# Performance work log

Measured on AMD Instinct MI355X. Metric: run time of the kernel, lower is better.

Reference implementation:

```python
import jax, jax.numpy as jnp
import numpy as np

NUM_HEADS = 12
ROPE_THETA = 100.0

def _rotate_half(x):
    x1 = x[..., ::2]
    x2 = x[..., 1::2]
    return jnp.stack((-x2, x1), axis=-1).reshape(x.shape)

def _apply_rope(x, cos, sin):
    return x * cos + _rotate_half(x) * sin

def _rope_cos_sin(h, w, head_dim, theta):
    quarter = head_dim // 4  # head_dim=64 -> 16 freq bands
    inv_freq = 1.0 / theta ** (jnp.arange(quarter, dtype=jnp.float32) / max(quarter, 1))
    y = jnp.repeat(jnp.arange(h, dtype=jnp.float32), w)   # [h*w]
    xc = jnp.tile(jnp.arange(w, dtype=jnp.float32), h)    # [h*w]
    y_freqs = y[:, None] * inv_freq[None, :]               # [N, quarter]
    x_freqs = xc[:, None] * inv_freq[None, :]
    y_ang = jnp.repeat(y_freqs, 2, axis=-1)                # [N, half]
    x_ang = jnp.repeat(x_freqs, 2, axis=-1)
    ang = jnp.concatenate([y_ang, x_ang], axis=-1)         # [N, head_dim]
    return jnp.cos(ang)[None, None], jnp.sin(ang)[None, None]  # [1,1,N,hd]

def setup_inputs() -> dict:
    key = jax.random.key(0)
    ks = jax.random.split(key, 8)
    B, S, D = 8, 1025, 768
    s = 0.02
    return {
        "x": jax.random.normal(ks[0], (B, S, D), jnp.float32),
        "q_w": jax.random.normal(ks[1], (D, D), jnp.float32) * s,
        "q_b": jax.random.normal(ks[2], (D,), jnp.float32) * s,
        "k_w": jax.random.normal(ks[3], (D, D), jnp.float32) * s,
        "v_w": jax.random.normal(ks[4], (D, D), jnp.float32) * s,
        "v_b": jax.random.normal(ks[5], (D,), jnp.float32) * s,
        "o_w": jax.random.normal(ks[6], (D, D), jnp.float32) * s,
        "o_b": jax.random.normal(ks[7], (D,), jnp.float32) * s,
        "h": 32,
        "w": 32,
        "num_prefix_tokens": 1,
    }

def reference(x, q_w, q_b, k_w, v_w, v_b, o_w, o_b, h, w, num_prefix_tokens):
    B, S, D = x.shape
    H = NUM_HEADS
    hd = D // H
    scale = hd ** -0.5
    p = num_prefix_tokens

    def proj(W, b):
        y = jnp.einsum('bsd,ed->bse', x, W)
        if b is not None:
            y = y + b
        return y.reshape(B, S, H, hd).transpose(0, 2, 1, 3)  # [B,H,S,hd]

    q = proj(q_w, q_b)
    k = proj(k_w, None)
    v = proj(v_w, v_b)

    cos, sin = _rope_cos_sin(h, w, hd, ROPE_THETA)
    q = jnp.concatenate([q[:, :, :p], _apply_rope(q[:, :, p:], cos, sin)], axis=2)
    k = jnp.concatenate([k[:, :, :p], _apply_rope(k[:, :, p:], cos, sin)], axis=2)

    attn = jnp.einsum('bhqd,bhkd->bhqk', q * scale, k)
    attn = jax.nn.softmax(attn, axis=-1)
    out = jnp.einsum('bhqk,bhkd->bhqd', attn, v)
    out = out.transpose(0, 2, 1, 3).reshape(B, S, D)
    return jnp.einsum('bsd,ed->bse', out, o_w) + o_b
```

## Files before the change

kernel.cpp:

```cpp
#include <hip/hip_runtime.h>

typedef unsigned short u16;
typedef unsigned int   u32;
typedef __attribute__((ext_vector_type(4))) short s4;
typedef __attribute__((ext_vector_type(8))) short s8;
typedef __attribute__((ext_vector_type(4))) float f4;
typedef __attribute__((ext_vector_type(16))) float f16v;

#define NB   8
#define SEQ  1025
#define DIM  768
#define NH   12
#define HD   64
#define BPAD 1040
#define MPAD 8320
#define MV   8200
#define SQP  1040
#define SKP  1088
#define NG16 68
#define NQKV 2304
#define BHT  96
#define QSCALE 0.1803368801111204f

__device__ __forceinline__ u16 f2bf(float f) {
  u32 u = __builtin_bit_cast(u32, f);
  u += 0x7fffu + ((u >> 16) & 1u);
  return (u16)(u >> 16);
}
__device__ __forceinline__ float bf2f(u16 h) {
  return __builtin_bit_cast(float, ((u32)h) << 16);
}
__device__ __forceinline__ float exp2f_(float x) {
#if __has_builtin(__builtin_amdgcn_exp2f)
  return __builtin_amdgcn_exp2f(x);
#else
  return exp2f(x);
#endif
}
__device__ __forceinline__ u32 cvtpk(float a, float b) {
  u32 r;
  asm("v_cvt_pk_bf16_f32 %0, %1, %2" : "=v"(r) : "v"(a), "v"(b));
  return r;
}

typedef const __attribute__((address_space(1))) void cas1v;
typedef __attribute__((address_space(3))) void as3v;
__device__ __forceinline__ void gload16(const void* g, void* l) {
  __builtin_amdgcn_global_load_lds((cas1v*)g, (as3v*)l, 16, 0, 0);
}

#define MFMA16(a, b, c) __builtin_amdgcn_mfma_f32_16x16x32_bf16(a, b, c, 0, 0, 0)
#define MFMA32(a, b, c) __builtin_amdgcn_mfma_f32_32x32x16_bf16(a, b, c, 0, 0, 0)

__global__ void conv_all(const float* __restrict__ x,
                         const float* __restrict__ qw, const float* __restrict__ kw,
                         const float* __restrict__ vw, const float* __restrict__ ow,
                         const float* __restrict__ qb, const float* __restrict__ vb,
                         u16* __restrict__ xb,
                         u16* __restrict__ wqkv, u16* __restrict__ wo,
                         float* __restrict__ biasq, float2* __restrict__ rt) {
  if (blockIdx.x < 6240) {
    int i = blockIdx.x * 256 + threadIdx.x;
    int e = i * 4;
    int row = e / DIM, col = e - row * DIM;
    int b = row / BPAD, s = row - b * BPAD;
    s4 o;
    if (s < SEQ) {
      float4 v = *(const float4*)(x + ((size_t)(b * SEQ + s)) * DIM + col);
      o[0] = (short)f2bf(v.x); o[1] = (short)f2bf(v.y);
      o[2] = (short)f2bf(v.z); o[3] = (short)f2bf(v.w);
    } else {
      o = (s4){0, 0, 0, 0};
    }
    *(s4*)(xb + e) = o;
  } else {
    int i = (blockIdx.x - 6240) * 256 + threadIdx.x;
    wqkv[i]           = f2bf(qw[i]);
    wqkv[i + 589824]  = f2bf(kw[i]);
    wqkv[i + 1179648] = f2bf(vw[i]);
    wo[i]             = f2bf(ow[i]);
    if (i < NQKV) biasq[i] = (i < 768) ? qb[i] : (i < 1536 ? 0.f : vb[i - 1536]);
    if (i < SEQ * 32) {
      int s = i >> 5, jj = i & 31;
      float cs = 1.f, sn = 0.f;
      if (s > 0) {
        int tok = s - 1;
        int pos = (jj < 16) ? (tok >> 5) : (tok & 31);
        int f = jj & 15;
        float ang = (float)pos * __expf((float)f * -0.28782313662425572f);
        __sincosf(ang, &sn, &cs);
      }
      rt[i] = make_float2(cs, sn);
    }
  }
}

__global__ __launch_bounds__(512, 4) void gemm_qkv(const u16* __restrict__ A, const u16* __restrict__ Bm,
                                                   const float* __restrict__ bias,
                                                   u16* __restrict__ Ql, u16* __restrict__ Kl,
                                                   u16* __restrict__ Vp, const float2* __restrict__ rt) {
  __shared__ u16 smem[24576];
  const int K = DIM;
  int tid = threadIdx.x;
  int lane = tid & 63, wave = tid >> 6;
  int g = lane >> 4, c16 = lane & 15;
  int wm = wave >> 2, wn = wave & 3;
  int nwg = gridDim.x, orig = blockIdx.x;
  int qd = nwg >> 3, rm = nwg & 7, xcd = orig & 7;
  int wgid = (xcd < rm ? xcd * (qd + 1) : rm * (qd + 1) + (xcd - rm) * qd) + (orig >> 3);
  int m0 = (wgid / 9) * 128, n0 = (wgid % 9) * 256;
  f4 acc[4][4] = {};

  int ldrow = wave * 16 + (lane >> 2);
  int ldk = ((lane & 3) ^ ((ldrow >> 1) & 3)) * 8;
  const u16* Asrc = A + (size_t)(m0 + ldrow) * K + ldk;
  const u16* Bsrc = Bm + (size_t)(n0 + ldrow) * K + ldk;

  auto stage = [&](int buf, int k0) {
    gload16(Asrc + k0,           smem + buf * 4096 + wave * 512);
    gload16(Bsrc + k0,           smem + 8192 + buf * 8192 + wave * 512);
    gload16(Bsrc + 128 * K + k0, smem + 8192 + buf * 8192 + 4096 + wave * 512);
  };

  stage(0, 0);
  __syncthreads();
  int kx = (g ^ ((c16 >> 1) & 3)) * 8;
  for (int t = 0; t < 24; t++) {
    int buf = t & 1;
    if (t + 1 < 24) stage(buf ^ 1, (t + 1) << 5);
    s8 af[4], bf[4];
#pragma unroll
    for (int i = 0; i < 4; i++) {
      af[i] = *(const s8*)(smem + buf * 4096 + (wm * 64 + i * 16 + c16) * 32 + kx);
      bf[i] = *(const s8*)(smem + 8192 + buf * 8192 + (wn * 64 + i * 16 + c16) * 32 + kx);
    }
    __builtin_amdgcn_s_setprio(1);
#pragma unroll
    for (int i = 0; i < 4; i++)
#pragma unroll
      for (int j = 0; j < 4; j++)
        acc[i][j] = MFMA16(af[i], bf[j], acc[i][j]);
    __builtin_amdgcn_s_setprio(0);
    __syncthreads();
  }

  int part = (n0 >= 1536) ? 2 : (n0 >= 768 ? 1 : 0);
  float qs = (part == 0) ? QSCALE : 1.0f;
  u16 (*ct)[258] = (u16(*)[258])smem;
#pragma unroll
  for (int ih = 0; ih < 2; ih++) {
    __syncthreads();
#pragma unroll
    for (int j = 0; j < 4; j++) {
      int col = wn * 64 + j * 16 + c16;
      float bv = bias[n0 + col];
      int jj = (col & 63) >> 1;
      int odd = col & 1;
#pragma unroll
      for (int il = 0; il < 2; il++) {
        int i = ih * 2 + il;
        int lrow = wm * 32 + il * 16 + g * 4;
        int mrow = m0 + wm * 64 + i * 16 + g * 4;
#pragma unroll
        for (int r = 0; r < 4; r++) {
          float v = acc[i][j][r] + bv;
          u16 o;
          if (part < 2) {
            float vp = __shfl_xor(v, 1);
            int s = (mrow + r) % BPAD;
            float2 t = rt[(s < SEQ ? s : SEQ - 1) * 32 + jj];
            float rv = odd ? (v * t.x + vp * t.y) : (v * t.x - vp * t.y);
            o = f2bf(rv * qs);
          } else {
            o = f2bf(v);
          }
          ct[lrow + r][col] = o;
        }
      }
    }
    __syncthreads();
    if (part < 2) {
      u16* dstB = (part == 0) ? Ql : Kl;
      int stride = (part == 0) ? SQP : SKP;
#pragma unroll
      for (int p = 0; p < 4; p++) {
        int task = p * 512 + tid;
        int lrow = task >> 5, cg = (task & 31) * 8;
        int m = m0 + (lrow >> 5) * 64 + ih * 32 + (lrow & 31);
        int b = m / BPAD, s = m - b * BPAD;
        int n = n0 + cg;
        int hq = (n >> 6) - part * NH;
        s8 v = *(const s8*)&ct[lrow][cg];
        *(s8*)(dstB + ((size_t)((b * NH + hq) * stride + s)) * HD + (n & 63)) = v;
      }
    } else {
#pragma unroll
      for (int p = 0; p < 2; p++) {
        int task = p * 512 + tid;
        int col = task & 255, rg = task >> 8;
        int lbase = rg * 16;
        int mb = m0 + (lbase >> 5) * 64 + ih * 32 + (lbase & 31);
        int b = mb / BPAD, sb = mb - b * BPAD;
        int g16 = sb >> 4;
        int n = n0 + col;
        int hq = (n >> 6) - 2 * NH;
        s8 o0, o1;
#pragma unroll
        for (int k = 0; k < 16; k++) {
          int mp = (k & 3) | (((k >> 3) & 1) << 2) | (((k >> 2) & 1) << 3);
          u16 val = ct[lbase + k][col];
          if (mp < 8) o0[mp] = (short)val; else o1[mp - 8] = (short)val;
        }
        u16* dst = Vp + ((size_t)((b * NH + hq) * NG16 + g16) * HD + (n & 63)) * 16;
        *(s8*)dst = o0;
        *(s8*)(dst + 8) = o1;
      }
    }
  }
}

__global__ __launch_bounds__(512, 4) void gemm_o(const u16* __restrict__ A, const u16* __restrict__ Bm,
                                                 float* __restrict__ Cf, const float* __restrict__ bias) {
  __shared__ u16 smem[24576];
  const int K = DIM;
  int tid = threadIdx.x;
  int lane = tid & 63, wave = tid >> 6;
  int g = lane >> 4, c16 = lane & 15;
  int wm = wave >> 2, wn = wave & 3;
  int nwg = gridDim.x, orig = blockIdx.x;
  int qd = nwg >> 3, rm = nwg & 7, xcd = orig & 7;
  int wgid = (xcd < rm ? xcd * (qd + 1) : rm * (qd + 1) + (xcd - rm) * qd) + (orig >> 3);
  int m0 = (wgid / 3) * 128, n0 = (wgid % 3) * 256;
  f4 acc[4][4] = {};

  int ldrow = wave * 16 + (lane >> 2);
  int ldk = ((lane & 3) ^ ((ldrow >> 1) & 3)) * 8;
  const u16* Asrc = A + (size_t)(m0 + ldrow) * K + ldk;
  const u16* Bsrc = Bm + (size_t)(n0 + ldrow) * K + ldk;

  auto stage = [&](int buf, int k0) {
    gload16(Asrc + k0,           smem + buf * 4096 + wave * 512);
    gload16(Bsrc + k0,           smem + 8192 + buf * 8192 + wave * 512);
    gload16(Bsrc + 128 * K + k0, smem + 8192 + buf * 8192 + 4096 + wave * 512);
  };

  stage(0, 0);
  __syncthreads();
  int kx = (g ^ ((c16 >> 1) & 3)) * 8;
  for (int t = 0; t < 24; t++) {
    int buf = t & 1;
    if (t + 1 < 24) stage(buf ^ 1, (t + 1) << 5);
    s8 af[4], bf[4];
#pragma unroll
    for (int i = 0; i < 4; i++) {
      af[i] = *(const s8*)(smem + buf * 4096 + (wm * 64 + i * 16 + c16) * 32 + kx);
      bf[i] = *(const s8*)(smem + 8192 + buf * 8192 + (wn * 64 + i * 16 + c16) * 32 + kx);
    }
    __builtin_amdgcn_s_setprio(1);
#pragma unroll
    for (int i = 0; i < 4; i++)
#pragma unroll
      for (int j = 0; j < 4; j++)
        acc[i][j] = MFMA16(af[i], bf[j], acc[i][j]);
    __builtin_amdgcn_s_setprio(0);
    __syncthreads();
  }

#pragma unroll
  for (int j = 0; j < 4; j++) {
    int n = n0 + wn * 64 + j * 16 + c16;
    float bv = bias[n];
#pragma unroll
    for (int i = 0; i < 4; i++) {
#pragma unroll
      for (int r = 0; r < 4; r++) {
        int m = m0 + wm * 64 + i * 16 + g * 4 + r;
        if (m < MV) Cf[(size_t)m * DIM + n] = acc[i][j][r] + bv;
      }
    }
  }
}

__global__ __launch_bounds__(512) void attn_k(const u16* __restrict__ Q, const u16* __restrict__ K,
                                              const u16* __restrict__ Vp, u16* __restrict__ Ao) {
  __shared__ u16 lds[2][64 * 64];
  int bh = blockIdx.x;
  int tid = threadIdx.x;
  int wave = tid >> 6, lane = tid & 63;
  int q32 = lane & 31, h = lane >> 5;
  int b = bh / NH, hh = bh % NH;
  int qb = blockIdx.y * 256 + wave * 32;
  if (qb > SEQ - 32) qb = SEQ - 32;
  const u16* Qb = Q + (size_t)bh * SQP * HD;
  const u16* Kb = K + (size_t)bh * SKP * HD;
  const u16* Vb = Vp + (size_t)bh * NG16 * 1024 + 16 * q32 + 8 * h;

  s8 qf[4];
#pragma unroll
  for (int t = 0; t < 4; t++)
    qf[t] = *(const s8*)(Qb + (size_t)(qb + q32) * HD + 16 * t + 8 * h);

  f16v o0 = {}, o1 = {};
  float lrun = 0.f;
  int swz = (q32 & 7) << 4;

  auto stage = [&](int buf, int c) {
    int row = tid >> 3;
    int ch = tid & 7;
    int so = (ch ^ (row & 7)) * 8;
    u16* kd = &lds[buf][tid * 8];
    gload16(Kb + (size_t)(c * 64 + row) * HD + so, kd);
  };

  stage(0, 0);
  __syncthreads();

  for (int c = 0; c < 17; c++) {
    int buf = c & 1;
    s8 vf0[4], vf1[4];
    {
      const u16* vc = Vb + c * 4096;
#pragma unroll
      for (int s = 0; s < 4; s++) {
        vf0[s] = *(const s8*)(vc + 1024 * s);
        vf1[s] = *(const s8*)(vc + 1024 * s + 512);
      }
    }
    if (c < 16) stage(buf ^ 1, c + 1);
    const char* Ks = (const char*)&lds[buf][0];

    f16v st0 = {}, st1 = {};
    __builtin_amdgcn_s_setprio(1);
#pragma unroll
    for (int t = 0; t < 4; t++) {
      int off = (32 * t + 16 * h) ^ swz;
      s8 a0 = *(const s8*)(Ks + q32 * 128 + off);
      s8 a1 = *(const s8*)(Ks + (32 + q32) * 128 + off);
      st0 = MFMA32(a0, qf[t], st0);
      st1 = MFMA32(a1, qf[t], st1);
    }
    __builtin_amdgcn_s_setprio(0);

    if (c == 16) {
      st0[0] = h ? -3e38f : st0[0];
#pragma unroll
      for (int r = 1; r < 16; r++) st0[r] = -3e38f;
#pragma unroll
      for (int r = 0; r < 16; r++) st1[r] = -3e38f;
    }

    float sm[8];
#pragma unroll
    for (int r = 0; r < 16; r++) {
      st0[r] = exp2f_(st0[r]);
      st1[r] = exp2f_(st1[r]);
    }
#pragma unroll
    for (int r = 0; r < 8; r++) sm[r] = (st0[r] + st0[r + 8]) + (st1[r] + st1[r + 8]);
#pragma unroll
    for (int w = 4; w >= 1; w >>= 1)
#pragma unroll
      for (int r = 0; r < w; r++) sm[r] += sm[r + w];
    lrun += sm[0] + __shfl_xor(sm[0], 32);

    __builtin_amdgcn_s_setprio(1);
#pragma unroll
    for (int s = 0; s < 4; s++) {
      union { s8 v; u32 w[4]; } pa;
#pragma unroll
      for (int i = 0; i < 4; i++) {
        float plo = (s < 2) ? st0[8 * (s & 1) + 2 * i]     : st1[8 * (s & 1) + 2 * i];
        float phi = (s < 2) ? st0[8 * (s & 1) + 2 * i + 1] : st1[8 * (s & 1) + 2 * i + 1];
        pa.w[i] = cvtpk(plo, phi);
      }
      o0 = MFMA32(pa.v, vf0[s], o0);
      o1 = MFMA32(pa.v, vf1[s], o1);
    }
    __builtin_amdgcn_s_setprio(0);
    __syncthreads();
  }

  float rl = 1.0f / lrun;
#pragma unroll
  for (int r = 0; r < 16; r++) {
    int cr = (r & 3) + 8 * (r >> 2) + 4 * h;
    float sc = __shfl(rl, cr);
    u16* dst = Ao + (size_t)(b * SEQ + qb + cr) * DIM + hh * HD;
    dst[q32]      = f2bf(o0[r] * sc);
    dst[32 + q32] = f2bf(o1[r] * sc);
  }
}

extern "C" void kernel_launch(void* const* d_in, const int* in_sizes, int n_in,
                              void* d_out, int out_size, void* d_ws, size_t ws_size,
                              hipStream_t stream) {
  const float* x  = (const float*)d_in[0];
  const float* qw = (const float*)d_in[1];
  const float* qb = (const float*)d_in[2];
  const float* kw = (const float*)d_in[3];
  const float* vw = (const float*)d_in[4];
  const float* vb = (const float*)d_in[5];
  const float* ow = (const float*)d_in[6];
  const float* ob = (const float*)d_in[7];
  float* out = (float*)d_out;

  char* ws = (char*)d_ws;
  u16*    xb   = (u16*)(ws);
  u16*    wqkv = (u16*)(ws + 12779520);
  u16*    wo   = (u16*)(ws + 16318464);
  float*  bq   = (float*)(ws + 17498112);
  float2* rt   = (float2*)(ws + 17507328);
  u16*    Ql   = (u16*)(ws + 17769728);
  u16*    Kl   = (u16*)(ws + 30549248);
  u16*    Vp   = (u16*)(ws + 43918592);
  u16*    Ao   = xb;

  conv_all<<<8544, 256, 0, stream>>>(x, qw, kw, vw, ow, qb, vb, xb, wqkv, wo, bq, rt);
  gemm_qkv<<<585, 512, 0, stream>>>(xb, wqkv, bq, Ql, Kl, Vp, rt);
  attn_k<<<dim3(96, 5), 512, 0, stream>>>(Ql, Kl, Vp, Ao);
  gemm_o<<<195, 512, 0, stream>>>(Ao, wo, out, ob);
}
```

Baseline: 142.3 us.

## Load K tiles directly into registers with double-buffered prefetch, drop LDS staging

Removes the shared-memory double buffer for K in the attention kernel. Each wave now loads its K fragments straight from global memory into registers, prefetching the next chunk while computing the current one, and the loop is unrolled by two to swap register buffers. This eliminates the per-iteration __syncthreads and the LDS round trip. In exchange, every wave redundantly fetches the same K chunk from global/L2, and register pressure goes up.

```diff
diff --git a/kernel.cpp b/kernel.cpp
--- a/kernel.cpp
+++ b/kernel.cpp
@@ -283,7 +283,6 @@
 
 __global__ __launch_bounds__(512) void attn_k(const u16* __restrict__ Q, const u16* __restrict__ K,
                                               const u16* __restrict__ Vp, u16* __restrict__ Ao) {
-  __shared__ u16 lds[2][64 * 64];
   int bh = blockIdx.x;
   int tid = threadIdx.x;
   int wave = tid >> 6, lane = tid & 63;
@@ -292,7 +291,7 @@
   int qb = blockIdx.y * 256 + wave * 32;
   if (qb > SEQ - 32) qb = SEQ - 32;
   const u16* Qb = Q + (size_t)bh * SQP * HD;
-  const u16* Kb = K + (size_t)bh * SKP * HD;
+  const u16* Kb = K + (size_t)bh * SKP * HD + (size_t)q32 * HD + 8 * h;
   const u16* Vb = Vp + (size_t)bh * NG16 * 1024 + 16 * q32 + 8 * h;
 
   s8 qf[4];
@@ -302,42 +301,36 @@
 
   f16v o0 = {}, o1 = {};
   float lrun = 0.f;
-  int swz = (q32 & 7) << 4;
-
-  auto stage = [&](int buf, int c) {
-    int row = tid >> 3;
-    int ch = tid & 7;
-    int so = (ch ^ (row & 7)) * 8;
-    u16* kd = &lds[buf][tid * 8];
-    gload16(Kb + (size_t)(c * 64 + row) * HD + so, kd);
-  };
-
-  stage(0, 0);
-  __syncthreads();
-
-  for (int c = 0; c < 17; c++) {
-    int buf = c & 1;
+
+  s8 ka0[4], ka1[4], kb0[4], kb1[4];
+#pragma unroll
+  for (int t = 0; t < 4; t++) {
+    ka0[t] = *(const s8*)(Kb + 16 * t);
+    ka1[t] = *(const s8*)(Kb + 32 * HD + 16 * t);
+  }
+
+  auto body = [&](int c, s8 (&k0)[4], s8 (&k1)[4], s8 (&n0)[4], s8 (&n1)[4]) {
+    const u16* vc = Vb + c * 4096;
     s8 vf0[4], vf1[4];
-    {
-      const u16* vc = Vb + c * 4096;
-#pragma unroll
-      for (int s = 0; s < 4; s++) {
-        vf0[s] = *(const s8*)(vc + 1024 * s);
-        vf1[s] = *(const s8*)(vc + 1024 * s + 512);
-      }
-    }
-    if (c < 16) stage(buf ^ 1, c + 1);
-    const char* Ks = (const char*)&lds[buf][0];
-
+#pragma unroll
+    for (int s = 0; s < 4; s++) {
+      vf0[s] = *(const s8*)(vc + 1024 * s);
+      vf1[s] = *(const s8*)(vc + 1024 * s + 512);
+    }
+    if (c < 16) {
+      const u16* kn = Kb + (size_t)(c + 1) * 64 * HD;
+#pragma unroll
+      for (int t = 0; t < 4; t++) {
+        n0[t] = *(const s8*)(kn + 16 * t);
+        n1[t] = *(const s8*)(kn + 32 * HD + 16 * t);
+      }
+    }
     f16v st0 = {}, st1 = {};
     __builtin_amdgcn_s_setprio(1);
 #pragma unroll
     for (int t = 0; t < 4; t++) {
-      int off = (32 * t + 16 * h) ^ swz;
-      s8 a0 = *(const s8*)(Ks + q32 * 128 + off);
-      s8 a1 = *(const s8*)(Ks + (32 + q32) * 128 + off);
-      st0 = MFMA32(a0, qf[t], st0);
-      st1 = MFMA32(a1, qf[t], st1);
+      st0 = MFMA32(k0[t], qf[t], st0);
+      st1 = MFMA32(k1[t], qf[t], st1);
     }
     __builtin_amdgcn_s_setprio(0);
 
@@ -377,8 +370,13 @@
       o1 = MFMA32(pa.v, vf1[s], o1);
     }
     __builtin_amdgcn_s_setprio(0);
-    __syncthreads();
-  }
+  };
+
+  for (int cc = 0; cc < 16; cc += 2) {
+    body(cc,     ka0, ka1, kb0, kb1);
+    body(cc + 1, kb0, kb1, ka0, ka1);
+  }
+  body(16, ka0, ka1, kb0, kb1);
 
   float rl = 1.0f / lrun;
 #pragma unroll
```

Result: slower. 177.0 us (+24.4%).
